# Kernel tuning notes

Measured on AMD Instinct MI355X. Metric: run time of the kernel, lower is better.

Reference implementation:

```python
import jax, jax.numpy as jnp
import numpy as np

O, A, H, L = 32, 8, 256, 3   # obs_units, act_units, hidden_units, hidden_layers
SCALE = 1.0                  # obs_scale
N, W = 512, 128              # n obs/action rows, n hypernet weight samples
W_TOTAL = (O*H + H) + (A*H + H) + (2*H*H + H) + L*(H*H + H) + (H*O + O) + (H + 1) + (H + 1)  # 348194


def _unpack(w):
    # Slice the flat per-sample weight vector exactly as PrimaryNetwork.feedforward does.
    c = [0]
    def take(n, shape=None):
        s = w[:, c[0]:c[0]+n]
        c[0] += n
        return s.reshape((w.shape[0],) + shape) if shape is not None else s
    w_obs = take(O*H, (H, O)); b_obs = take(H)
    w_act = take(A*H, (H, A)); b_act = take(H)
    w_tgt = take(2*H*H, (H, 2*H)); b_tgt = take(H)
    ws, bs = [], []
    for _ in range(L):
        ws.append(take(H*H, (H, H))); bs.append(take(H))
    w_state = take(H*O, (O, H)); b_state = take(O)
    w_reward = take(H, (1, H)); b_reward = take(1)
    w_done = take(H, (1, H)); b_done = take(1)
    return w_obs, b_obs, w_act, b_act, w_tgt, b_tgt, ws, bs, w_state, b_state, w_reward, b_reward, w_done, b_done


def setup_inputs() -> dict:
    key = jax.random.key(0)
    k1, k2, k3 = jax.random.split(key, 3)
    return {
        "obs": jax.random.normal(k1, (N, O), jnp.float32),
        "action": jax.random.normal(k2, (N, A), jnp.float32),
        # scale ~1/sqrt(H) so activations stay in a sane range through the MLP
        "w": jax.random.normal(k3, (W, W_TOTAL), jnp.float32) * (1.0 / np.sqrt(H)),
        "obs_min": jnp.zeros((O,), jnp.float32),
        "obs_max": jnp.ones((O,), jnp.float32),
    }


def reference(obs, action, w, obs_min, obs_max):
    lrelu = jax.nn.leaky_relu  # negative_slope=0.01, matches F.leaky_relu default
    (w_obs, b_obs, w_act, b_act, w_tgt, b_tgt, ws, bs,
     w_state, b_state, w_reward, b_reward, w_done, b_done) = _unpack(w)

    # normalize obs to [-scale, scale]
    x = (obs - obs_min[None, :]) / (obs_max - obs_min)[None, :]
    x = (2.0 * x - 1.0) * SCALE                         # [N, O]

    # per-sample hypernetwork MLP, batched over (N obs rows) x (W weight samples)
    o = jnp.einsum('who,no->nwh', w_obs, x) + b_obs[None]          # [N, W, H]
    a = jnp.einsum('wha,na->nwh', w_act, action) + b_act[None]     # [N, W, H]
    y = lrelu(jnp.concatenate([o, a], axis=-1))                    # [N, W, 2H]
    y = lrelu(jnp.einsum('whk,nwk->nwh', w_tgt, y) + b_tgt[None])  # [N, W, H]
    for wj, bj in zip(ws, bs):
        y = lrelu(jnp.einsum('whk,nwk->nwh', wj, y) + bj[None])

    next_states = jnp.einsum('wok,nwk->nwo', w_state, y) + b_state[None] + x[:, None, :]  # [N, W, O]
    rewards = jnp.tanh(jnp.einsum('wok,nwk->nwo', w_reward, y) + b_reward[None])          # [N, W, 1]
    dones = jax.nn.sigmoid(jnp.einsum('wok,nwk->nwo', w_done, y) + b_done[None])          # [N, W, 1]

    # un-normalize next_states
    next_states = (next_states / SCALE + 1.0) * 0.5
    next_states = next_states * (obs_max - obs_min)[None, None, :] + obs_min[None, None, :]
    return next_states, rewards, dones
```

## Files before the change

### kernel.cpp

```cpp
#include <hip/hip_runtime.h>
#include <cstdint>
#include <cstddef>

#define SCALE_F 1.0f
#define NMEM    128
#define WTOTAL  348194

#define OFF_WOBS   0
#define OFF_BOBS   8192
#define OFF_WACT   8448
#define OFF_BACT   10496
#define OFF_WTGT   10752
#define OFF_BTGT   141824
#define OFF_WS0    142080
#define OFF_BS0    207616
#define OFF_WS1    207872
#define OFF_BS1    273408
#define OFF_WS2    273664
#define OFF_BS2    339200
#define OFF_WSTATE 339456
#define OFF_BSTATE 347648
#define OFF_WREW   347680
#define OFF_BREW   347936
#define OFF_WDONE  347937
#define OFF_BDONE  348193

#define OUT_REW  2097152
#define OUT_DONE 2162688

#define RB 128

#define APITCH 264
#define XPITCH 72

typedef __attribute__((ext_vector_type(8))) short short8;
typedef __attribute__((ext_vector_type(4))) float f32x4;

__device__ __forceinline__ uint16_t f2b(float f) {
  union { float f; uint32_t u; } x;
  x.f = f;
  uint32_t u = x.u + 0x7fffu + ((x.u >> 16) & 1u);
  return (uint16_t)(u >> 16);
}

__device__ __forceinline__ void zero8(f32x4 acc[8]) {
#pragma unroll
  for (int r = 0; r < 8; ++r)
#pragma unroll
    for (int j = 0; j < 4; ++j) acc[r][j] = 0.0f;
}

__device__ __forceinline__ void accum_k8(f32x4 acc[8], const uint16_t* Abase,
                                         const float* wrow) {
  float2 f[8][4];
#pragma unroll
  for (int kt = 0; kt < 8; ++kt)
#pragma unroll
    for (int i = 0; i < 4; ++i)
      f[kt][i] = reinterpret_cast<const float2*>(wrow + kt * 32)[i];

#pragma unroll
  for (int kt = 0; kt < 8; ++kt) {
    short8 b;
#pragma unroll
    for (int i = 0; i < 4; ++i) {
      b[2 * i]     = (short)f2b(f[kt][i].x);
      b[2 * i + 1] = (short)f2b(f[kt][i].y);
    }
#pragma unroll
    for (int rt = 0; rt < 8; ++rt) {
      const short8 a =
          *reinterpret_cast<const short8*>(Abase + rt * 16 * APITCH + kt * 32);
      acc[rt] = __builtin_amdgcn_mfma_f32_16x16x32_bf16(a, b, acc[rt], 0, 0, 0);
    }
  }
}

__device__ __forceinline__ void epi_lrelu(const f32x4 acc[8], float bv,
                                          uint16_t* Bout, int c, int lg) {
#pragma unroll
  for (int rt = 0; rt < 8; ++rt) {
#pragma unroll
    for (int j = 0; j < 4; ++j) {
      float v = acc[rt][j] + bv;
      v = (v > 0.0f) ? v : 0.01f * v;
      Bout[(rt * 16 + lg * 4 + j) * APITCH + c] = f2b(v);
    }
  }
}

__global__ void __launch_bounds__(1024, 4)
pn_kernel(const float* __restrict__ obs, const float* __restrict__ action,
          const float* __restrict__ w, const float* __restrict__ omin,
          const float* __restrict__ omax, float* __restrict__ out)
{
  __shared__ __align__(16) uint16_t xa[RB * XPITCH];
  __shared__ __align__(16) uint16_t B1[RB * APITCH];
  __shared__ __align__(16) uint16_t B2[RB * APITCH];

  const int tid  = threadIdx.x;
  const int lane = tid & 63;
  const int wid  = tid >> 6;
  const int lr   = lane & 15;
  const int lg   = lane >> 4;
  const int c    = wid * 16 + lr;

  const int bid    = blockIdx.x;
  const int xcd    = bid & 7;
  const int j5     = bid >> 3;
  const int member = xcd * 16 + (j5 >> 2);
  const int chunk  = j5 & 3;
  const int n0     = chunk * RB;
  const float* wm  = w + (size_t)member * WTOTAL;

  {
    const int row = tid >> 3, seg = tid & 7;
    const int n = n0 + row;
    float v[8];
    if (seg < 4) {
      const int c0 = seg * 8;
#pragma unroll
      for (int i = 0; i < 8; ++i) {
        const float mn = omin[c0 + i], mx = omax[c0 + i];
        v[i] = (2.0f * (obs[n * 32 + c0 + i] - mn) / (mx - mn) - 1.0f) * SCALE_F;
      }
    } else if (seg == 4) {
#pragma unroll
      for (int i = 0; i < 8; ++i) v[i] = action[n * 8 + i];
    } else {
#pragma unroll
      for (int i = 0; i < 8; ++i) v[i] = 0.0f;
    }
    short8 s;
#pragma unroll
    for (int i = 0; i < 8; ++i) s[i] = (short)f2b(v[i]);
    *reinterpret_cast<short8*>(xa + row * XPITCH + seg * 8) = s;
  }
  __syncthreads();

  {
    f32x4 acc[8];
    zero8(acc);
    float2 f[4];
#pragma unroll
    for (int i = 0; i < 4; ++i)
      f[i] = reinterpret_cast<const float2*>(wm + OFF_WOBS + c * 32 + lg * 8)[i];
    short8 b;
#pragma unroll
    for (int i = 0; i < 4; ++i) {
      b[2 * i] = (short)f2b(f[i].x);
      b[2 * i + 1] = (short)f2b(f[i].y);
    }
#pragma unroll
    for (int rt = 0; rt < 8; ++rt) {
      const short8 a =
          *reinterpret_cast<const short8*>(xa + (rt * 16 + lr) * XPITCH + lg * 8);
      acc[rt] = __builtin_amdgcn_mfma_f32_16x16x32_bf16(a, b, acc[rt], 0, 0, 0);
    }
    epi_lrelu(acc, wm[OFF_BOBS + c], B1, c, lg);
  }

  {
    f32x4 acc[8];
    zero8(acc);
    float2 f[4];
#pragma unroll
    for (int i = 0; i < 4; ++i)
      f[i] = reinterpret_cast<const float2*>(wm + OFF_WACT + c * 8 + lg * 8)[i];
    short8 b;
#pragma unroll
    for (int i = 0; i < 4; ++i) {
      b[2 * i] = (short)f2b(f[i].x);
      b[2 * i + 1] = (short)f2b(f[i].y);
    }
#pragma unroll
    for (int rt = 0; rt < 8; ++rt) {
      const short8 a = *reinterpret_cast<const short8*>(
          xa + (rt * 16 + lr) * XPITCH + 32 + lg * 8);
      acc[rt] = __builtin_amdgcn_mfma_f32_16x16x32_bf16(a, b, acc[rt], 0, 0, 0);
    }
    epi_lrelu(acc, wm[OFF_BACT + c], B2, c, lg);
  }
  __syncthreads();

  {
    f32x4 acc[8];
    zero8(acc);
    accum_k8(acc, B1 + lr * APITCH + lg * 8, wm + OFF_WTGT + c * 512 + lg * 8);
    __syncthreads();
    accum_k8(acc, B2 + lr * APITCH + lg * 8,
             wm + OFF_WTGT + c * 512 + 256 + lg * 8);
    epi_lrelu(acc, wm[OFF_BTGT + c], B1, c, lg);
  }
  __syncthreads();

  {
    f32x4 acc[8];
    zero8(acc);
    accum_k8(acc, B1 + lr * APITCH + lg * 8, wm + OFF_WS0 + c * 256 + lg * 8);
    epi_lrelu(acc, wm[OFF_BS0 + c], B2, c, lg);
  }
  __syncthreads();

  {
    f32x4 acc[8];
    zero8(acc);
    accum_k8(acc, B2 + lr * APITCH + lg * 8, wm + OFF_WS1 + c * 256 + lg * 8);
    epi_lrelu(acc, wm[OFF_BS1 + c], B1, c, lg);
  }
  __syncthreads();

  {
    f32x4 acc[8];
    zero8(acc);
    accum_k8(acc, B1 + lr * APITCH + lg * 8, wm + OFF_WS2 + c * 256 + lg * 8);
    epi_lrelu(acc, wm[OFF_BS2 + c], B2, c, lg);
  }
  __syncthreads();

  if (wid < 3) {
    f32x4 acc[8];
    zero8(acc);
#pragma unroll
    for (int kt = 0; kt < 8; ++kt) {
      short8 b;
      if (c < 32) {
        const float* p = wm + OFF_WSTATE + c * 256 + kt * 32 + lg * 8;
#pragma unroll
        for (int i = 0; i < 4; ++i) {
          float2 t = reinterpret_cast<const float2*>(p)[i];
          b[2 * i] = (short)f2b(t.x);
          b[2 * i + 1] = (short)f2b(t.y);
        }
      } else if (c == 32) {
        const float* p = wm + OFF_WREW + kt * 32 + lg * 8;
#pragma unroll
        for (int i = 0; i < 4; ++i) {
          float2 t = reinterpret_cast<const float2*>(p)[i];
          b[2 * i] = (short)f2b(t.x);
          b[2 * i + 1] = (short)f2b(t.y);
        }
      } else if (c == 33) {
        const float* p = wm + OFF_WDONE + kt * 32 + lg * 8;
#pragma unroll
        for (int i = 0; i < 8; ++i) b[i] = (short)f2b(p[i]);
      } else {
#pragma unroll
        for (int i = 0; i < 8; ++i) b[i] = 0;
      }
#pragma unroll
      for (int rt = 0; rt < 8; ++rt) {
        const short8 a = *reinterpret_cast<const short8*>(
            B2 + (rt * 16 + lr) * APITCH + kt * 32 + lg * 8);
        acc[rt] = __builtin_amdgcn_mfma_f32_16x16x32_bf16(a, b, acc[rt], 0, 0, 0);
      }
    }

    if (c < 34) {
#pragma unroll
      for (int rt = 0; rt < 8; ++rt) {
#pragma unroll
        for (int j = 0; j < 4; ++j) {
          const int n = n0 + rt * 16 + lg * 4 + j;
          float v = acc[rt][j];
          if (c < 32) {
            const float mn = omin[c], mx = omax[c];
            const float rng = mx - mn;
            const float x =
                (2.0f * (obs[n * 32 + c] - mn) / rng - 1.0f) * SCALE_F;
            v += wm[OFF_BSTATE + c] + x;
            v = (v / SCALE_F + 1.0f) * 0.5f;
            out[((size_t)n * NMEM + member) * 32 + c] = v * rng + mn;
          } else if (c == 32) {
            v += wm[OFF_BREW];
            out[(size_t)OUT_REW + n * NMEM + member] = tanhf(v);
          } else {
            v += wm[OFF_BDONE];
            out[(size_t)OUT_DONE + n * NMEM + member] = 1.0f / (1.0f + expf(-v));
          }
        }
      }
    }
  }
}

extern "C" void kernel_launch(void* const* d_in, const int* in_sizes, int n_in,
                              void* d_out, int out_size, void* d_ws, size_t ws_size,
                              hipStream_t stream) {
  (void)in_sizes; (void)n_in; (void)out_size; (void)d_ws; (void)ws_size;
  const float* obs    = (const float*)d_in[0];
  const float* action = (const float*)d_in[1];
  const float* w      = (const float*)d_in[2];
  const float* omin   = (const float*)d_in[3];
  const float* omax   = (const float*)d_in[4];
  float* out = (float*)d_out;

  pn_kernel<<<dim3(512), dim3(1024), 0, stream>>>(obs, action, w, omin, omax, out);
}
```

Before: 130.3 us.

## Halve block to 512 threads, two column tiles per wave, single LDS buffer

Each wave now computes two 16-column output tiles, so every A fragment read from LDS feeds two MFMAs. The block shrinks from 1024 to 512 threads and the two ping-pong activation buffers become one, with an extra barrier between accumulate and epilogue. The input staging buffer is removed: obs and action fragments are built straight from global memory in registers. The fp32-to-bf16 conversion is replaced by a cheaper packed perm-based rounding that does not do round-to-nearest-even on ties. The cost is higher register pressure from doubled accumulators, and fewer waves to hide weight-load latency.

```diff
diff --git a/kernel.cpp b/kernel.cpp
--- a/kernel.cpp
+++ b/kernel.cpp
@@ -2,7 +2,6 @@
 #include <cstdint>
 #include <cstddef>
 
-#define SCALE_F 1.0f
 #define NMEM    128
 #define WTOTAL  348194
 
@@ -29,81 +28,91 @@
 #define OUT_DONE 2162688
 
 #define RB 128
-
 #define APITCH 264
-#define XPITCH 72
 
 typedef __attribute__((ext_vector_type(8))) short short8;
 typedef __attribute__((ext_vector_type(4))) float f32x4;
 
-__device__ __forceinline__ uint16_t f2b(float f) {
-  union { float f; uint32_t u; } x;
-  x.f = f;
-  uint32_t u = x.u + 0x7fffu + ((x.u >> 16) & 1u);
-  return (uint16_t)(u >> 16);
-}
-
-__device__ __forceinline__ void zero8(f32x4 acc[8]) {
-#pragma unroll
-  for (int r = 0; r < 8; ++r)
-#pragma unroll
-    for (int j = 0; j < 4; ++j) acc[r][j] = 0.0f;
-}
-
-__device__ __forceinline__ void accum_k8(f32x4 acc[8], const uint16_t* Abase,
-                                         const float* wrow) {
-  float2 f[8][4];
-#pragma unroll
-  for (int kt = 0; kt < 8; ++kt)
-#pragma unroll
-    for (int i = 0; i < 4; ++i)
-      f[kt][i] = reinterpret_cast<const float2*>(wrow + kt * 32)[i];
-
+__device__ __forceinline__ uint32_t pkbf2(float lo, float hi) {
+  union { float f; uint32_t u; } a, b;
+  a.f = lo; b.f = hi;
+  return __builtin_amdgcn_perm(b.u + 0x8000u, a.u + 0x8000u, 0x07060302u);
+}
+
+__device__ __forceinline__ uint16_t f2b_fast(float f) {
+  union { float f; uint32_t u; } x; x.f = f;
+  return (uint16_t)((x.u + 0x8000u) >> 16);
+}
+
+__device__ __forceinline__ short8 pk8(const float2 f[4]) {
+  union { uint32_t u[4]; short8 s; } r;
+#pragma unroll
+  for (int i = 0; i < 4; ++i) r.u[i] = pkbf2(f[i].x, f[i].y);
+  return r.s;
+}
+
+__device__ __forceinline__ void zero_acc(f32x4 a0[8], f32x4 a1[8]) {
+#pragma unroll
+  for (int r = 0; r < 8; ++r) {
+#pragma unroll
+    for (int j = 0; j < 4; ++j) { a0[r][j] = 0.0f; a1[r][j] = 0.0f; }
+  }
+}
+
+__device__ __forceinline__ void accum_pass(f32x4 acc0[8], f32x4 acc1[8],
+                                           const uint16_t* __restrict__ Ab,
+                                           const float* __restrict__ w0,
+                                           const float* __restrict__ w1) {
 #pragma unroll
   for (int kt = 0; kt < 8; ++kt) {
-    short8 b;
-#pragma unroll
-    for (int i = 0; i < 4; ++i) {
-      b[2 * i]     = (short)f2b(f[kt][i].x);
-      b[2 * i + 1] = (short)f2b(f[kt][i].y);
-    }
+    float2 f0[4], f1[4];
+#pragma unroll
+    for (int i = 0; i < 4; ++i) f0[i] = reinterpret_cast<const float2*>(w0 + kt * 32)[i];
+#pragma unroll
+    for (int i = 0; i < 4; ++i) f1[i] = reinterpret_cast<const float2*>(w1 + kt * 32)[i];
+    const short8 b0 = pk8(f0);
+    const short8 b1 = pk8(f1);
 #pragma unroll
     for (int rt = 0; rt < 8; ++rt) {
       const short8 a =
-          *reinterpret_cast<const short8*>(Abase + rt * 16 * APITCH + kt * 32);
-      acc[rt] = __builtin_amdgcn_mfma_f32_16x16x32_bf16(a, b, acc[rt], 0, 0, 0);
-    }
-  }
-}
-
-__device__ __forceinline__ void epi_lrelu(const f32x4 acc[8], float bv,
-                                          uint16_t* Bout, int c, int lg) {
+          *reinterpret_cast<const short8*>(Ab + rt * 16 * APITCH + kt * 32);
+      acc0[rt] = __builtin_amdgcn_mfma_f32_16x16x32_bf16(a, b0, acc0[rt], 0, 0, 0);
+      acc1[rt] = __builtin_amdgcn_mfma_f32_16x16x32_bf16(a, b1, acc1[rt], 0, 0, 0);
+    }
+  }
+}
+
+__device__ __forceinline__ void epi2(const f32x4 acc0[8], const f32x4 acc1[8],
+                                     float b0, float b1,
+                                     uint16_t* __restrict__ B, int ct0, int ct1,
+                                     int lg) {
 #pragma unroll
   for (int rt = 0; rt < 8; ++rt) {
 #pragma unroll
     for (int j = 0; j < 4; ++j) {
-      float v = acc[rt][j] + bv;
-      v = (v > 0.0f) ? v : 0.01f * v;
-      Bout[(rt * 16 + lg * 4 + j) * APITCH + c] = f2b(v);
-    }
-  }
-}
-
-__global__ void __launch_bounds__(1024, 4)
+      const int row = rt * 16 + lg * 4 + j;
+      float v0 = acc0[rt][j] + b0; v0 = (v0 > 0.0f) ? v0 : 0.01f * v0;
+      float v1 = acc1[rt][j] + b1; v1 = (v1 > 0.0f) ? v1 : 0.01f * v1;
+      B[row * APITCH + ct0] = f2b_fast(v0);
+      B[row * APITCH + ct1] = f2b_fast(v1);
+    }
+  }
+}
+
+__global__ void __launch_bounds__(512, 4)
 pn_kernel(const float* __restrict__ obs, const float* __restrict__ action,
           const float* __restrict__ w, const float* __restrict__ omin,
           const float* __restrict__ omax, float* __restrict__ out)
 {
-  __shared__ __align__(16) uint16_t xa[RB * XPITCH];
   __shared__ __align__(16) uint16_t B1[RB * APITCH];
-  __shared__ __align__(16) uint16_t B2[RB * APITCH];
 
   const int tid  = threadIdx.x;
   const int lane = tid & 63;
   const int wid  = tid >> 6;
   const int lr   = lane & 15;
   const int lg   = lane >> 4;
-  const int c    = wid * 16 + lr;
+  const int ct0  = wid * 32 + lr;
+  const int ct1  = ct0 + 16;
 
   const int bid    = blockIdx.x;
   const int xcd    = bid & 7;
@@ -113,170 +122,198 @@
   const int n0     = chunk * RB;
   const float* wm  = w + (size_t)member * WTOTAL;
 
+  const uint16_t* Ab = B1 + lr * APITCH + lg * 8;
+
+  float sc[8], of[8];
+#pragma unroll
+  for (int i = 0; i < 8; ++i) {
+    const float mn = omin[lg * 8 + i], mx = omax[lg * 8 + i];
+    const float s = 2.0f / (mx - mn);
+    sc[i] = s;
+    of[i] = -mn * s - 1.0f;
+  }
+
   {
-    const int row = tid >> 3, seg = tid & 7;
-    const int n = n0 + row;
-    float v[8];
-    if (seg < 4) {
-      const int c0 = seg * 8;
-#pragma unroll
-      for (int i = 0; i < 8; ++i) {
-        const float mn = omin[c0 + i], mx = omax[c0 + i];
-        v[i] = (2.0f * (obs[n * 32 + c0 + i] - mn) / (mx - mn) - 1.0f) * SCALE_F;
-      }
-    } else if (seg == 4) {
-#pragma unroll
-      for (int i = 0; i < 8; ++i) v[i] = action[n * 8 + i];
-    } else {
-#pragma unroll
-      for (int i = 0; i < 8; ++i) v[i] = 0.0f;
-    }
-    short8 s;
-#pragma unroll
-    for (int i = 0; i < 8; ++i) s[i] = (short)f2b(v[i]);
-    *reinterpret_cast<short8*>(xa + row * XPITCH + seg * 8) = s;
-  }
+    float2 fb0[4], fb1[4];
+#pragma unroll
+    for (int i = 0; i < 4; ++i) {
+      fb0[i] = reinterpret_cast<const float2*>(wm + OFF_WOBS + ct0 * 32 + lg * 8)[i];
+      fb1[i] = reinterpret_cast<const float2*>(wm + OFF_WOBS + ct1 * 32 + lg * 8)[i];
+    }
+    const short8 b0 = pk8(fb0);
+    const short8 b1 = pk8(fb1);
+    const float bb0 = wm[OFF_BOBS + ct0], bb1 = wm[OFF_BOBS + ct1];
+#pragma unroll
+    for (int rt = 0; rt < 8; ++rt) {
+      const int n = n0 + rt * 16 + lr;
+      const float4 x0 = *reinterpret_cast<const float4*>(obs + n * 32 + lg * 8);
+      const float4 x1 = *reinterpret_cast<const float4*>(obs + n * 32 + lg * 8 + 4);
+      union { uint32_t u[4]; short8 s; } afr;
+      afr.u[0] = pkbf2(x0.x * sc[0] + of[0], x0.y * sc[1] + of[1]);
+      afr.u[1] = pkbf2(x0.z * sc[2] + of[2], x0.w * sc[3] + of[3]);
+      afr.u[2] = pkbf2(x1.x * sc[4] + of[4], x1.y * sc[5] + of[5]);
+      afr.u[3] = pkbf2(x1.z * sc[6] + of[6], x1.w * sc[7] + of[7]);
+      f32x4 a0 = {0.0f, 0.0f, 0.0f, 0.0f}, a1 = {0.0f, 0.0f, 0.0f, 0.0f};
+      a0 = __builtin_amdgcn_mfma_f32_16x16x32_bf16(afr.s, b0, a0, 0, 0, 0);
+      a1 = __builtin_amdgcn_mfma_f32_16x16x32_bf16(afr.s, b1, a1, 0, 0, 0);
+#pragma unroll
+      for (int j = 0; j < 4; ++j) {
+        float v0 = a0[j] + bb0; v0 = (v0 > 0.0f) ? v0 : 0.01f * v0;
+        float v1 = a1[j] + bb1; v1 = (v1 > 0.0f) ? v1 : 0.01f * v1;
+        B1[(rt * 16 + lg * 4 + j) * APITCH + ct0] = f2b_fast(v0);
+        B1[(rt * 16 + lg * 4 + j) * APITCH + ct1] = f2b_fast(v1);
+      }
+    }
+  }
+  __syncthreads();
+
+  f32x4 acc0[8], acc1[8];
+  zero_acc(acc0, acc1);
+
+  accum_pass(acc0, acc1, Ab, wm + OFF_WTGT + ct0 * 512 + lg * 8,
+                             wm + OFF_WTGT + ct1 * 512 + lg * 8);
   __syncthreads();
 
   {
-    f32x4 acc[8];
-    zero8(acc);
-    float2 f[4];
-#pragma unroll
-    for (int i = 0; i < 4; ++i)
-      f[i] = reinterpret_cast<const float2*>(wm + OFF_WOBS + c * 32 + lg * 8)[i];
-    short8 b;
+    float2 fb0[4], fb1[4];
 #pragma unroll
     for (int i = 0; i < 4; ++i) {
-      b[2 * i] = (short)f2b(f[i].x);
-      b[2 * i + 1] = (short)f2b(f[i].y);
-    }
+      fb0[i] = reinterpret_cast<const float2*>(wm + OFF_WACT + ct0 * 8 + lg * 8)[i];
+      fb1[i] = reinterpret_cast<const float2*>(wm + OFF_WACT + ct1 * 8 + lg * 8)[i];
+    }
+    const short8 b0 = pk8(fb0);
+    const short8 b1 = pk8(fb1);
+    const float bb0 = wm[OFF_BACT + ct0], bb1 = wm[OFF_BACT + ct1];
 #pragma unroll
     for (int rt = 0; rt < 8; ++rt) {
-      const short8 a =
-          *reinterpret_cast<const short8*>(xa + (rt * 16 + lr) * XPITCH + lg * 8);
-      acc[rt] = __builtin_amdgcn_mfma_f32_16x16x32_bf16(a, b, acc[rt], 0, 0, 0);
-    }
-    epi_lrelu(acc, wm[OFF_BOBS + c], B1, c, lg);
-  }
-
-  {
-    f32x4 acc[8];
-    zero8(acc);
-    float2 f[4];
-#pragma unroll
-    for (int i = 0; i < 4; ++i)
-      f[i] = reinterpret_cast<const float2*>(wm + OFF_WACT + c * 8 + lg * 8)[i];
-    short8 b;
-#pragma unroll
-    for (int i = 0; i < 4; ++i) {
-      b[2 * i] = (short)f2b(f[i].x);
-      b[2 * i + 1] = (short)f2b(f[i].y);
-    }
-#pragma unroll
-    for (int rt = 0; rt < 8; ++rt) {
-      const short8 a = *reinterpret_cast<const short8*>(
-          xa + (rt * 16 + lr) * XPITCH + 32 + lg * 8);
-      acc[rt] = __builtin_amdgcn_mfma_f32_16x16x32_bf16(a, b, acc[rt], 0, 0, 0);
-    }
-    epi_lrelu(acc, wm[OFF_BACT + c], B2, c, lg);
-  }
-  __syncthreads();
-
-  {
-    f32x4 acc[8];
-    zero8(acc);
-    accum_k8(acc, B1 + lr * APITCH + lg * 8, wm + OFF_WTGT + c * 512 + lg * 8);
-    __syncthreads();
-    accum_k8(acc, B2 + lr * APITCH + lg * 8,
-             wm + OFF_WTGT + c * 512 + 256 + lg * 8);
-    epi_lrelu(acc, wm[OFF_BTGT + c], B1, c, lg);
-  }
-  __syncthreads();
-
-  {
-    f32x4 acc[8];
-    zero8(acc);
-    accum_k8(acc, B1 + lr * APITCH + lg * 8, wm + OFF_WS0 + c * 256 + lg * 8);
-    epi_lrelu(acc, wm[OFF_BS0 + c], B2, c, lg);
-  }
-  __syncthreads();
-
-  {
-    f32x4 acc[8];
-    zero8(acc);
-    accum_k8(acc, B2 + lr * APITCH + lg * 8, wm + OFF_WS1 + c * 256 + lg * 8);
-    epi_lrelu(acc, wm[OFF_BS1 + c], B1, c, lg);
-  }
-  __syncthreads();
-
-  {
-    f32x4 acc[8];
-    zero8(acc);
-    accum_k8(acc, B1 + lr * APITCH + lg * 8, wm + OFF_WS2 + c * 256 + lg * 8);
-    epi_lrelu(acc, wm[OFF_BS2 + c], B2, c, lg);
-  }
-  __syncthreads();
-
-  if (wid < 3) {
-    f32x4 acc[8];
-    zero8(acc);
+      const int n = n0 + rt * 16 + lr;
+      union { uint32_t u[4]; short8 s; } afr;
+      if (lg == 0) {
+        const float4 q0 = *reinterpret_cast<const float4*>(action + n * 8);
+        const float4 q1 = *reinterpret_cast<const float4*>(action + n * 8 + 4);
+        afr.u[0] = pkbf2(q0.x, q0.y);
+        afr.u[1] = pkbf2(q0.z, q0.w);
+        afr.u[2] = pkbf2(q1.x, q1.y);
+        afr.u[3] = pkbf2(q1.z, q1.w);
+      } else {
+        afr.u[0] = afr.u[1] = afr.u[2] = afr.u[3] = 0u;
+      }
+      f32x4 a0 = {0.0f, 0.0f, 0.0f, 0.0f}, a1 = {0.0f, 0.0f, 0.0f, 0.0f};
+      a0 = __builtin_amdgcn_mfma_f32_16x16x32_bf16(afr.s, b0, a0, 0, 0, 0);
+      a1 = __builtin_amdgcn_mfma_f32_16x16x32_bf16(afr.s, b1, a1, 0, 0, 0);
+#pragma unroll
+      for (int j = 0; j < 4; ++j) {
+        float v0 = a0[j] + bb0; v0 = (v0 > 0.0f) ? v0 : 0.01f * v0;
+        float v1 = a1[j] + bb1; v1 = (v1 > 0.0f) ? v1 : 0.01f * v1;
+        B1[(rt * 16 + lg * 4 + j) * APITCH + ct0] = f2b_fast(v0);
+        B1[(rt * 16 + lg * 4 + j) * APITCH + ct1] = f2b_fast(v1);
+      }
+    }
+  }
+  __syncthreads();
+
+  accum_pass(acc0, acc1, Ab, wm + OFF_WTGT + ct0 * 512 + 256 + lg * 8,
+                             wm + OFF_WTGT + ct1 * 512 + 256 + lg * 8);
+  __syncthreads();
+  epi2(acc0, acc1, wm[OFF_BTGT + ct0], wm[OFF_BTGT + ct1], B1, ct0, ct1, lg);
+  __syncthreads();
+
+  zero_acc(acc0, acc1);
+  accum_pass(acc0, acc1, Ab, wm + OFF_WS0 + ct0 * 256 + lg * 8,
+                             wm + OFF_WS0 + ct1 * 256 + lg * 8);
+  __syncthreads();
+  epi2(acc0, acc1, wm[OFF_BS0 + ct0], wm[OFF_BS0 + ct1], B1, ct0, ct1, lg);
+  __syncthreads();
+
+  zero_acc(acc0, acc1);
+  accum_pass(acc0, acc1, Ab, wm + OFF_WS1 + ct0 * 256 + lg * 8,
+                             wm + OFF_WS1 + ct1 * 256 + lg * 8);
+  __syncthreads();
+  epi2(acc0, acc1, wm[OFF_BS1 + ct0], wm[OFF_BS1 + ct1], B1, ct0, ct1, lg);
+  __syncthreads();
+
+  zero_acc(acc0, acc1);
+  accum_pass(acc0, acc1, Ab, wm + OFF_WS2 + ct0 * 256 + lg * 8,
+                             wm + OFF_WS2 + ct1 * 256 + lg * 8);
+  __syncthreads();
+  epi2(acc0, acc1, wm[OFF_BS2 + ct0], wm[OFF_BS2 + ct1], B1, ct0, ct1, lg);
+  __syncthreads();
+
+  if (wid < 2) {
+    zero_acc(acc0, acc1);
 #pragma unroll
     for (int kt = 0; kt < 8; ++kt) {
-      short8 b;
-      if (c < 32) {
-        const float* p = wm + OFF_WSTATE + c * 256 + kt * 32 + lg * 8;
+      short8 b0, b1;
+      {
+        union { uint32_t u[4]; short8 s; } z;
+        z.u[0] = z.u[1] = z.u[2] = z.u[3] = 0u;
+        b0 = z.s; b1 = z.s;
+      }
+      if (wid == 0) {
+        float2 f0[4], f1[4];
 #pragma unroll
         for (int i = 0; i < 4; ++i) {
-          float2 t = reinterpret_cast<const float2*>(p)[i];
-          b[2 * i] = (short)f2b(t.x);
-          b[2 * i + 1] = (short)f2b(t.y);
+          f0[i] = reinterpret_cast<const float2*>(
+                      wm + OFF_WSTATE + ct0 * 256 + kt * 32 + lg * 8)[i];
+          f1[i] = reinterpret_cast<const float2*>(
+                      wm + OFF_WSTATE + ct1 * 256 + kt * 32 + lg * 8)[i];
         }
-      } else if (c == 32) {
-        const float* p = wm + OFF_WREW + kt * 32 + lg * 8;
-#pragma unroll
-        for (int i = 0; i < 4; ++i) {
-          float2 t = reinterpret_cast<const float2*>(p)[i];
-          b[2 * i] = (short)f2b(t.x);
-          b[2 * i + 1] = (short)f2b(t.y);
-        }
-      } else if (c == 33) {
+        b0 = pk8(f0);
+        b1 = pk8(f1);
+      } else if (lr == 0) {
+        float2 f0[4];
+#pragma unroll
+        for (int i = 0; i < 4; ++i)
+          f0[i] = reinterpret_cast<const float2*>(wm + OFF_WREW + kt * 32 + lg * 8)[i];
+        b0 = pk8(f0);
+      } else if (lr == 1) {
         const float* p = wm + OFF_WDONE + kt * 32 + lg * 8;
-#pragma unroll
-        for (int i = 0; i < 8; ++i) b[i] = (short)f2b(p[i]);
-      } else {
-#pragma unroll
-        for (int i = 0; i < 8; ++i) b[i] = 0;
+        union { uint32_t u[4]; short8 s; } r;
+#pragma unroll
+        for (int i = 0; i < 4; ++i) r.u[i] = pkbf2(p[2 * i], p[2 * i + 1]);
+        b0 = r.s;
       }
 #pragma unroll
       for (int rt = 0; rt < 8; ++rt) {
-        const short8 a = *reinterpret_cast<const short8*>(
-            B2 + (rt * 16 + lr) * APITCH + kt * 32 + lg * 8);
-        acc[rt] = __builtin_amdgcn_mfma_f32_16x16x32_bf16(a, b, acc[rt], 0, 0, 0);
-      }
-    }
-
-    if (c < 34) {
+        const short8 a =
+            *reinterpret_cast<const short8*>(Ab + rt * 16 * APITCH + kt * 32);
+        acc0[rt] = __builtin_amdgcn_mfma_f32_16x16x32_bf16(a, b0, acc0[rt], 0, 0, 0);
+        if (wid == 0)
+          acc1[rt] = __builtin_amdgcn_mfma_f32_16x16x32_bf16(a, b1, acc1[rt], 0, 0, 0);
+      }
+    }
+
+    if (wid == 0) {
+      const float mn0 = omin[ct0], rg0 = omax[ct0] - mn0;
+      const float mn1 = omin[ct1], rg1 = omax[ct1] - mn1;
+      const float bs0 = wm[OFF_BSTATE + ct0], bs1 = wm[OFF_BSTATE + ct1];
 #pragma unroll
       for (int rt = 0; rt < 8; ++rt) {
 #pragma unroll
         for (int j = 0; j < 4; ++j) {
           const int n = n0 + rt * 16 + lg * 4 + j;
-          float v = acc[rt][j];
-          if (c < 32) {
-            const float mn = omin[c], mx = omax[c];
-            const float rng = mx - mn;
-            const float x =
-                (2.0f * (obs[n * 32 + c] - mn) / rng - 1.0f) * SCALE_F;
-            v += wm[OFF_BSTATE + c] + x;
-            v = (v / SCALE_F + 1.0f) * 0.5f;
-            out[((size_t)n * NMEM + member) * 32 + c] = v * rng + mn;
-          } else if (c == 32) {
-            v += wm[OFF_BREW];
-            out[(size_t)OUT_REW + n * NMEM + member] = tanhf(v);
-          } else {
-            v += wm[OFF_BDONE];
-            out[(size_t)OUT_DONE + n * NMEM + member] = 1.0f / (1.0f + expf(-v));
+          const float x0 = 2.0f * (obs[n * 32 + ct0] - mn0) / rg0 - 1.0f;
+          const float x1 = 2.0f * (obs[n * 32 + ct1] - mn1) / rg1 - 1.0f;
+          float v0 = acc0[rt][j] + bs0 + x0;
+          float v1 = acc1[rt][j] + bs1 + x1;
+          v0 = (v0 + 1.0f) * 0.5f;
+          v1 = (v1 + 1.0f) * 0.5f;
+          out[((size_t)n * NMEM + member) * 32 + ct0] = v0 * rg0 + mn0;
+          out[((size_t)n * NMEM + member) * 32 + ct1] = v1 * rg1 + mn1;
+        }
+      }
+    } else {
+      const float br = wm[OFF_BREW], bd = wm[OFF_BDONE];
+#pragma unroll
+      for (int rt = 0; rt < 8; ++rt) {
+#pragma unroll
+        for (int j = 0; j < 4; ++j) {
+          const int n = n0 + rt * 16 + lg * 4 + j;
+          if (lr == 0) {
+            out[(size_t)OUT_REW + (size_t)n * NMEM + member] = tanhf(acc0[rt][j] + br);
+          } else if (lr == 1) {
+            out[(size_t)OUT_DONE + (size_t)n * NMEM + member] =
+                1.0f / (1.0f + expf(-(acc0[rt][j] + bd)));
           }
         }
       }
@@ -295,5 +332,5 @@
   const float* omax   = (const float*)d_in[4];
   float* out = (float*)d_out;
 
-  pn_kernel<<<dim3(512), dim3(1024), 0, stream>>>(obs, action, w, omin, omax, out);
-}
+  pn_kernel<<<dim3(512), dim3(512), 0, stream>>>(obs, action, w, omin, omax, out);
+}
```

Result: slower. 276.1 us (+111.8%).

## Collapse activation buffers to a single LDS tile and stream weight loads

Applied to the files above, without the earlier changes.

Removes the xa staging buffer and second activation buffer, keeping all layers in one shared tile with extra barriers between read and overwrite phases. The input layers now build their A fragments straight from global obs/action, and the second half of the target layer is computed after the action layer overwrites the same buffer. Weight prefetch in the K loop becomes double-buffered per k-step instead of loading all eight at once, which cuts register pressure. Launch bounds are raised to 8 for occupancy, and bf16 conversion switches to a cheaper round-half-up packed perm, which changes rounding slightly. The cost is more block-wide syncs.

```diff
diff --git a/kernel.cpp b/kernel.cpp
--- a/kernel.cpp
+++ b/kernel.cpp
@@ -2,7 +2,6 @@
 #include <cstdint>
 #include <cstddef>
 
-#define SCALE_F 1.0f
 #define NMEM    128
 #define WTOTAL  348194
 
@@ -29,18 +28,27 @@
 #define OUT_DONE 2162688
 
 #define RB 128
-
 #define APITCH 264
-#define XPITCH 72
 
 typedef __attribute__((ext_vector_type(8))) short short8;
 typedef __attribute__((ext_vector_type(4))) float f32x4;
 
-__device__ __forceinline__ uint16_t f2b(float f) {
-  union { float f; uint32_t u; } x;
-  x.f = f;
-  uint32_t u = x.u + 0x7fffu + ((x.u >> 16) & 1u);
-  return (uint16_t)(u >> 16);
+__device__ __forceinline__ uint32_t pkbf2(float lo, float hi) {
+  union { float f; uint32_t u; } a, b;
+  a.f = lo; b.f = hi;
+  return __builtin_amdgcn_perm(b.u + 0x8000u, a.u + 0x8000u, 0x07060302u);
+}
+
+__device__ __forceinline__ uint16_t f2b_fast(float f) {
+  union { float f; uint32_t u; } x; x.f = f;
+  return (uint16_t)((x.u + 0x8000u) >> 16);
+}
+
+__device__ __forceinline__ short8 pk8(const float2 f[4]) {
+  union { uint32_t u[4]; short8 s; } r;
+#pragma unroll
+  for (int i = 0; i < 4; ++i) r.u[i] = pkbf2(f[i].x, f[i].y);
+  return r.s;
 }
 
 __device__ __forceinline__ void zero8(f32x4 acc[8]) {
@@ -50,53 +58,51 @@
     for (int j = 0; j < 4; ++j) acc[r][j] = 0.0f;
 }
 
-__device__ __forceinline__ void accum_k8(f32x4 acc[8], const uint16_t* Abase,
-                                         const float* wrow) {
-  float2 f[8][4];
-#pragma unroll
-  for (int kt = 0; kt < 8; ++kt)
-#pragma unroll
-    for (int i = 0; i < 4; ++i)
-      f[kt][i] = reinterpret_cast<const float2*>(wrow + kt * 32)[i];
-
+__device__ __forceinline__ void accum_k8(f32x4 acc[8],
+                                         const uint16_t* __restrict__ Ab,
+                                         const float* __restrict__ wrow) {
+  float2 f[2][4];
+#pragma unroll
+  for (int i = 0; i < 4; ++i)
+    f[0][i] = reinterpret_cast<const float2*>(wrow)[i];
 #pragma unroll
   for (int kt = 0; kt < 8; ++kt) {
-    short8 b;
-#pragma unroll
-    for (int i = 0; i < 4; ++i) {
-      b[2 * i]     = (short)f2b(f[kt][i].x);
-      b[2 * i + 1] = (short)f2b(f[kt][i].y);
-    }
+    if (kt < 7) {
+#pragma unroll
+      for (int i = 0; i < 4; ++i)
+        f[(kt + 1) & 1][i] =
+            reinterpret_cast<const float2*>(wrow + (kt + 1) * 32)[i];
+    }
+    const short8 b = pk8(f[kt & 1]);
 #pragma unroll
     for (int rt = 0; rt < 8; ++rt) {
       const short8 a =
-          *reinterpret_cast<const short8*>(Abase + rt * 16 * APITCH + kt * 32);
+          *reinterpret_cast<const short8*>(Ab + rt * 16 * APITCH + kt * 32);
       acc[rt] = __builtin_amdgcn_mfma_f32_16x16x32_bf16(a, b, acc[rt], 0, 0, 0);
     }
   }
 }
 
 __device__ __forceinline__ void epi_lrelu(const f32x4 acc[8], float bv,
-                                          uint16_t* Bout, int c, int lg) {
+                                          uint16_t* __restrict__ B, int c,
+                                          int lg) {
 #pragma unroll
   for (int rt = 0; rt < 8; ++rt) {
 #pragma unroll
     for (int j = 0; j < 4; ++j) {
       float v = acc[rt][j] + bv;
       v = (v > 0.0f) ? v : 0.01f * v;
-      Bout[(rt * 16 + lg * 4 + j) * APITCH + c] = f2b(v);
-    }
-  }
-}
-
-__global__ void __launch_bounds__(1024, 4)
+      B[(rt * 16 + lg * 4 + j) * APITCH + c] = f2b_fast(v);
+    }
+  }
+}
+
+__global__ void __launch_bounds__(1024, 8)
 pn_kernel(const float* __restrict__ obs, const float* __restrict__ action,
           const float* __restrict__ w, const float* __restrict__ omin,
           const float* __restrict__ omax, float* __restrict__ out)
 {
-  __shared__ __align__(16) uint16_t xa[RB * XPITCH];
   __shared__ __align__(16) uint16_t B1[RB * APITCH];
-  __shared__ __align__(16) uint16_t B2[RB * APITCH];
 
   const int tid  = threadIdx.x;
   const int lane = tid & 63;
@@ -113,145 +119,139 @@
   const int n0     = chunk * RB;
   const float* wm  = w + (size_t)member * WTOTAL;
 
+  const uint16_t* Ab = B1 + lr * APITCH + lg * 8;
+
   {
-    const int row = tid >> 3, seg = tid & 7;
-    const int n = n0 + row;
-    float v[8];
-    if (seg < 4) {
-      const int c0 = seg * 8;
-#pragma unroll
-      for (int i = 0; i < 8; ++i) {
-        const float mn = omin[c0 + i], mx = omax[c0 + i];
-        v[i] = (2.0f * (obs[n * 32 + c0 + i] - mn) / (mx - mn) - 1.0f) * SCALE_F;
-      }
-    } else if (seg == 4) {
-#pragma unroll
-      for (int i = 0; i < 8; ++i) v[i] = action[n * 8 + i];
-    } else {
-#pragma unroll
-      for (int i = 0; i < 8; ++i) v[i] = 0.0f;
-    }
-    short8 s;
-#pragma unroll
-    for (int i = 0; i < 8; ++i) s[i] = (short)f2b(v[i]);
-    *reinterpret_cast<short8*>(xa + row * XPITCH + seg * 8) = s;
-  }
+    float sc[8], of[8];
+#pragma unroll
+    for (int i = 0; i < 8; ++i) {
+      const float mn = omin[lg * 8 + i], mx = omax[lg * 8 + i];
+      const float s = 2.0f / (mx - mn);
+      sc[i] = s;
+      of[i] = -mn * s - 1.0f;
+    }
+    float2 fb[4];
+#pragma unroll
+    for (int i = 0; i < 4; ++i)
+      fb[i] = reinterpret_cast<const float2*>(wm + OFF_WOBS + c * 32 + lg * 8)[i];
+    const short8 b = pk8(fb);
+    const float bb = wm[OFF_BOBS + c];
+#pragma unroll
+    for (int rt = 0; rt < 8; ++rt) {
+      const int n = n0 + rt * 16 + lr;
+      const float4 x0 = *reinterpret_cast<const float4*>(obs + n * 32 + lg * 8);
+      const float4 x1 = *reinterpret_cast<const float4*>(obs + n * 32 + lg * 8 + 4);
+      union { uint32_t u[4]; short8 s; } afr;
+      afr.u[0] = pkbf2(x0.x * sc[0] + of[0], x0.y * sc[1] + of[1]);
+      afr.u[1] = pkbf2(x0.z * sc[2] + of[2], x0.w * sc[3] + of[3]);
+      afr.u[2] = pkbf2(x1.x * sc[4] + of[4], x1.y * sc[5] + of[5]);
+      afr.u[3] = pkbf2(x1.z * sc[6] + of[6], x1.w * sc[7] + of[7]);
+      f32x4 a0 = {0.0f, 0.0f, 0.0f, 0.0f};
+      a0 = __builtin_amdgcn_mfma_f32_16x16x32_bf16(afr.s, b, a0, 0, 0, 0);
+#pragma unroll
+      for (int j = 0; j < 4; ++j) {
+        float v = a0[j] + bb;
+        v = (v > 0.0f) ? v : 0.01f * v;
+        B1[(rt * 16 + lg * 4 + j) * APITCH + c] = f2b_fast(v);
+      }
+    }
+  }
+  __syncthreads();
+
+  f32x4 acc[8];
+  zero8(acc);
+
+  accum_k8(acc, Ab, wm + OFF_WTGT + c * 512 + lg * 8);
   __syncthreads();
 
   {
-    f32x4 acc[8];
-    zero8(acc);
-    float2 f[4];
+    float2 fb[4];
 #pragma unroll
     for (int i = 0; i < 4; ++i)
-      f[i] = reinterpret_cast<const float2*>(wm + OFF_WOBS + c * 32 + lg * 8)[i];
-    short8 b;
-#pragma unroll
-    for (int i = 0; i < 4; ++i) {
-      b[2 * i] = (short)f2b(f[i].x);
-      b[2 * i + 1] = (short)f2b(f[i].y);
-    }
+      fb[i] = reinterpret_cast<const float2*>(wm + OFF_WACT + c * 8 + lg * 8)[i];
+    const short8 b = pk8(fb);
+    const float bb = wm[OFF_BACT + c];
 #pragma unroll
     for (int rt = 0; rt < 8; ++rt) {
-      const short8 a =
-          *reinterpret_cast<const short8*>(xa + (rt * 16 + lr) * XPITCH + lg * 8);
-      acc[rt] = __builtin_amdgcn_mfma_f32_16x16x32_bf16(a, b, acc[rt], 0, 0, 0);
-    }
-    epi_lrelu(acc, wm[OFF_BOBS + c], B1, c, lg);
-  }
-
-  {
-    f32x4 acc[8];
-    zero8(acc);
-    float2 f[4];
-#pragma unroll
-    for (int i = 0; i < 4; ++i)
-      f[i] = reinterpret_cast<const float2*>(wm + OFF_WACT + c * 8 + lg * 8)[i];
-    short8 b;
-#pragma unroll
-    for (int i = 0; i < 4; ++i) {
-      b[2 * i] = (short)f2b(f[i].x);
-      b[2 * i + 1] = (short)f2b(f[i].y);
-    }
-#pragma unroll
-    for (int rt = 0; rt < 8; ++rt) {
-      const short8 a = *reinterpret_cast<const short8*>(
-          xa + (rt * 16 + lr) * XPITCH + 32 + lg * 8);
-      acc[rt] = __builtin_amdgcn_mfma_f32_16x16x32_bf16(a, b, acc[rt], 0, 0, 0);
-    }
-    epi_lrelu(acc, wm[OFF_BACT + c], B2, c, lg);
-  }
-  __syncthreads();
-
-  {
-    f32x4 acc[8];
-    zero8(acc);
-    accum_k8(acc, B1 + lr * APITCH + lg * 8, wm + OFF_WTGT + c * 512 + lg * 8);
-    __syncthreads();
-    accum_k8(acc, B2 + lr * APITCH + lg * 8,
-             wm + OFF_WTGT + c * 512 + 256 + lg * 8);
-    epi_lrelu(acc, wm[OFF_BTGT + c], B1, c, lg);
-  }
-  __syncthreads();
-
-  {
-    f32x4 acc[8];
-    zero8(acc);
-    accum_k8(acc, B1 + lr * APITCH + lg * 8, wm + OFF_WS0 + c * 256 + lg * 8);
-    epi_lrelu(acc, wm[OFF_BS0 + c], B2, c, lg);
-  }
-  __syncthreads();
-
-  {
-    f32x4 acc[8];
-    zero8(acc);
-    accum_k8(acc, B2 + lr * APITCH + lg * 8, wm + OFF_WS1 + c * 256 + lg * 8);
-    epi_lrelu(acc, wm[OFF_BS1 + c], B1, c, lg);
-  }
-  __syncthreads();
-
-  {
-    f32x4 acc[8];
-    zero8(acc);
-    accum_k8(acc, B1 + lr * APITCH + lg * 8, wm + OFF_WS2 + c * 256 + lg * 8);
-    epi_lrelu(acc, wm[OFF_BS2 + c], B2, c, lg);
-  }
+      const int n = n0 + rt * 16 + lr;
+      union { uint32_t u[4]; short8 s; } afr;
+      if (lg == 0) {
+        const float4 q0 = *reinterpret_cast<const float4*>(action + n * 8);
+        const float4 q1 = *reinterpret_cast<const float4*>(action + n * 8 + 4);
+        afr.u[0] = pkbf2(q0.x, q0.y);
+        afr.u[1] = pkbf2(q0.z, q0.w);
+        afr.u[2] = pkbf2(q1.x, q1.y);
+        afr.u[3] = pkbf2(q1.z, q1.w);
+      } else {
+        afr.u[0] = afr.u[1] = afr.u[2] = afr.u[3] = 0u;
+      }
+      f32x4 a0 = {0.0f, 0.0f, 0.0f, 0.0f};
+      a0 = __builtin_amdgcn_mfma_f32_16x16x32_bf16(afr.s, b, a0, 0, 0, 0);
+#pragma unroll
+      for (int j = 0; j < 4; ++j) {
+        float v = a0[j] + bb;
+        v = (v > 0.0f) ? v : 0.01f * v;
+        B1[(rt * 16 + lg * 4 + j) * APITCH + c] = f2b_fast(v);
+      }
+    }
+  }
+  __syncthreads();
+
+  accum_k8(acc, Ab, wm + OFF_WTGT + c * 512 + 256 + lg * 8);
+  __syncthreads();
+  epi_lrelu(acc, wm[OFF_BTGT + c], B1, c, lg);
+  __syncthreads();
+
+  zero8(acc);
+  accum_k8(acc, Ab, wm + OFF_WS0 + c * 256 + lg * 8);
+  __syncthreads();
+  epi_lrelu(acc, wm[OFF_BS0 + c], B1, c, lg);
+  __syncthreads();
+
+  zero8(acc);
+  accum_k8(acc, Ab, wm + OFF_WS1 + c * 256 + lg * 8);
+  __syncthreads();
+  epi_lrelu(acc, wm[OFF_BS1 + c], B1, c, lg);
+  __syncthreads();
+
+  zero8(acc);
+  accum_k8(acc, Ab, wm + OFF_WS2 + c * 256 + lg * 8);
+  __syncthreads();
+  epi_lrelu(acc, wm[OFF_BS2 + c], B1, c, lg);
   __syncthreads();
 
   if (wid < 3) {
-    f32x4 acc[8];
     zero8(acc);
 #pragma unroll
     for (int kt = 0; kt < 8; ++kt) {
       short8 b;
       if (c < 32) {
         const float* p = wm + OFF_WSTATE + c * 256 + kt * 32 + lg * 8;
-#pragma unroll
-        for (int i = 0; i < 4; ++i) {
-          float2 t = reinterpret_cast<const float2*>(p)[i];
-          b[2 * i] = (short)f2b(t.x);
-          b[2 * i + 1] = (short)f2b(t.y);
-        }
+        float2 f[4];
+#pragma unroll
+        for (int i = 0; i < 4; ++i) f[i] = reinterpret_cast<const float2*>(p)[i];
+        b = pk8(f);
       } else if (c == 32) {
         const float* p = wm + OFF_WREW + kt * 32 + lg * 8;
-#pragma unroll
-        for (int i = 0; i < 4; ++i) {
-          float2 t = reinterpret_cast<const float2*>(p)[i];
-          b[2 * i] = (short)f2b(t.x);
-          b[2 * i + 1] = (short)f2b(t.y);
-        }
+        float2 f[4];
+#pragma unroll
+        for (int i = 0; i < 4; ++i) f[i] = reinterpret_cast<const float2*>(p)[i];
+        b = pk8(f);
       } else if (c == 33) {
         const float* p = wm + OFF_WDONE + kt * 32 + lg * 8;
-#pragma unroll
-        for (int i = 0; i < 8; ++i) b[i] = (short)f2b(p[i]);
+        union { uint32_t u[4]; short8 s; } r;
+#pragma unroll
+        for (int i = 0; i < 4; ++i) r.u[i] = pkbf2(p[2 * i], p[2 * i + 1]);
+        b = r.s;
       } else {
-#pragma unroll
-        for (int i = 0; i < 8; ++i) b[i] = 0;
+        union { uint32_t u[4]; short8 s; } z;
+        z.u[0] = z.u[1] = z.u[2] = z.u[3] = 0u;
+        b = z.s;
       }
 #pragma unroll
       for (int rt = 0; rt < 8; ++rt) {
-        const short8 a = *reinterpret_cast<const short8*>(
-            B2 + (rt * 16 + lr) * APITCH + kt * 32 + lg * 8);
+        const short8 a =
+            *reinterpret_cast<const short8*>(Ab + rt * 16 * APITCH + kt * 32);
         acc[rt] = __builtin_amdgcn_mfma_f32_16x16x32_bf16(a, b, acc[rt], 0, 0, 0);
       }
     }
@@ -266,17 +266,17 @@
           if (c < 32) {
             const float mn = omin[c], mx = omax[c];
             const float rng = mx - mn;
-            const float x =
-                (2.0f * (obs[n * 32 + c] - mn) / rng - 1.0f) * SCALE_F;
+            const float x = 2.0f * (obs[n * 32 + c] - mn) / rng - 1.0f;
             v += wm[OFF_BSTATE + c] + x;
-            v = (v / SCALE_F + 1.0f) * 0.5f;
+            v = (v + 1.0f) * 0.5f;
             out[((size_t)n * NMEM + member) * 32 + c] = v * rng + mn;
           } else if (c == 32) {
             v += wm[OFF_BREW];
-            out[(size_t)OUT_REW + n * NMEM + member] = tanhf(v);
+            out[(size_t)OUT_REW + (size_t)n * NMEM + member] = tanhf(v);
           } else {
             v += wm[OFF_BDONE];
-            out[(size_t)OUT_DONE + n * NMEM + member] = 1.0f / (1.0f + expf(-v));
+            out[(size_t)OUT_DONE + (size_t)n * NMEM + member] =
+                1.0f / (1.0f + expf(-v));
           }
         }
       }
```

Result: slower. 135.7 us (+4.1%).
